# Kernel optimization log

Hardware: AMD Instinct MI355X
Metric: run time of the kernel (lower is better)

## Reference

```python
import jax, jax.numpy as jnp
import numpy as np

B, DIM, H, W = 8, 64, 64, 64
N_EMBED = 512
NNZ = 4          # num_nonzero OMP iterations
REG = 1e-7       # tiny Tikhonov term for the batched normal-equation solves


def batch_omp(X, D, S):
    """Batch OMP: for each signal pick S atoms greedily and solve LS on support.
    X: [N, d] signals, D: [d, K] dictionary with unit-norm atoms.
    Returns dense sparse code [N, K] with <= S nonzeros per row.
    Mathematically equivalent to the incremental-Cholesky Batch_OMP: at each
    step we solve G_II gamma = alpha0_I on the current support I.
    """
    N, K = X.shape[0], D.shape[1]
    G = D.T @ D                 # [K, K] Gram matrix (precomputed once)
    alpha0 = X @ D              # [N, K] initial correlations D^T x
    alpha = alpha0
    idx_cols = []
    gamma = None
    idx = None
    for k in range(S):          # static small loop over sparsity level
        j = jnp.argmax(jnp.abs(alpha), axis=1)                # [N] greedy atom
        idx_cols.append(j)
        idx = jnp.stack(idx_cols, axis=1)                     # [N, k+1]
        G_sub = G[idx[:, :, None], idx[:, None, :]]           # [N, k+1, k+1]
        rhs = jnp.take_along_axis(alpha0, idx, axis=1)        # [N, k+1]
        reg = REG * jnp.eye(k + 1, dtype=G.dtype)
        gamma = jnp.linalg.solve(G_sub + reg, rhs[..., None])[..., 0]  # [N, k+1]
        # residual correlations: alpha = alpha0 - G[:, I] gamma  (G symmetric)
        alpha = alpha0 - jnp.einsum('nak,na->nk', G[idx], gamma)
    code = jnp.zeros((N, K), X.dtype).at[jnp.arange(N)[:, None], idx].set(gamma)
    return code


def setup_inputs() -> dict:
    key = jax.random.key(0)
    kx, kd = jax.random.split(key)
    x = jax.random.normal(kx, (B, DIM, H, W), dtype=jnp.float32)
    dictionary = jax.random.normal(kd, (DIM, N_EMBED), dtype=jnp.float32)
    return {"x": x, "dictionary": dictionary}


def reference(x, dictionary):
    perm = jnp.transpose(x, (0, 2, 3, 1))            # [B, H, W, C]
    flat = perm.reshape(-1, DIM)                     # [N, C], N = B*H*W
    # normalize_dict=True: atoms normalized to unit L2 norm (in-place in torch)
    Dn = dictionary / jnp.linalg.norm(dictionary, axis=0, keepdims=True)
    code = batch_omp(flat, Dn, NNZ)                  # [N, K] (torch keeps [K, N])
    quant = (code @ Dn.T).reshape(perm.shape)        # reconstruction
    diff_enc = jnp.mean((quant - perm) ** 2)
    diff_dict = diff_enc                             # backward_dict=False branch
    # straight-through: perm + (quant - perm).detach() == quant in value
    out = jnp.transpose(quant, (0, 3, 1, 2))         # [B, C, H, W]
    ids = jnp.transpose(code.reshape(B, H, W, N_EMBED), (0, 3, 1, 2))  # [B, K, H, W]
    norm_0 = jnp.sum(code != 0, axis=1).astype(jnp.float32)  # L0 per signal, [N]
    num_steps = jnp.float32(NNZ)
    mean_D = jnp.mean(jnp.abs(Dn))
    mean_Z = jnp.mean(jnp.abs(code))
    norm_Z = jnp.mean(norm_0)
    topk_num = max(1, int(norm_0.shape[0] * 0.01))   # static: 327
    top_percentile = jnp.min(jax.lax.top_k(norm_0, topk_num)[0])
    num_zeros = jnp.sum(norm_0 == 0).astype(jnp.float32)
    return (out, diff_enc, diff_dict, ids, num_steps, mean_D, mean_Z,
            norm_Z, top_percentile, num_zeros)
```

## Files before the change

### kernel.cpp

```cpp
#include <hip/hip_runtime.h>
#include <cstdint>
#include <cstddef>

#define BQ 8
#define CDIM 64
#define HQ 64
#define WQ 64
#define KDIM 512
#define N_SIG 32768
#define S_NNZ 4

#define DIFF_ENC_OFF 2097152
#define DIFF_DICT_OFF 2097153
#define IDS_OFF 2097154
#define NUM_STEPS_OFF 18874370
#define MEAN_D_OFF 18874371
#define MEAN_Z_OFF 18874372
#define NORM_Z_OFF 18874373
#define TOP_PCT_OFF 18874374
#define NUM_ZEROS_OFF 18874375

#define WS_DN 16
#define WS_DNT 32784
#define WS_G 65552
#define WS_WG 327696
#define WS_WI 458768

__global__ __launch_bounds__(512) void k_dict(const float* __restrict__ D,
                                              float* __restrict__ Dn,
                                              float* __restrict__ DnT,
                                              float* __restrict__ W) {
  int tid = threadIdx.x;
  if (tid < 16) ((unsigned int*)W)[tid] = 0u;
  __syncthreads();
  double* accs = (double*)W;
  int k = tid;
  float ss = 0.f;
  for (int c = 0; c < CDIM; ++c) {
    float v = D[c * KDIM + k];
    ss = fmaf(v, v, ss);
  }
  float nrm = sqrtf(ss);
  float sabs = 0.f;
  for (int c = 0; c < CDIM; ++c) {
    float v = D[c * KDIM + k] / nrm;
    Dn[c * KDIM + k] = v;
    DnT[k * CDIM + c] = v;
    sabs += fabsf(v);
  }
#pragma unroll
  for (int off = 32; off >= 1; off >>= 1) sabs += __shfl_xor(sabs, off);
  if ((tid & 63) == 0) atomicAdd(&accs[0], (double)sabs);
}

__global__ __launch_bounds__(256) void k_gram(const float* __restrict__ Dn,
                                              float* __restrict__ G) {
  int g = blockIdx.x * 256 + threadIdx.x;
  int i = g >> 9, j = g & 511;
  float s = 0.f;
#pragma unroll 8
  for (int c = 0; c < CDIM; ++c) s = fmaf(Dn[c * KDIM + i], Dn[c * KDIM + j], s);
  G[(size_t)i * KDIM + j] = s;
}

__global__ __launch_bounds__(256) void k_alpha0(const float* __restrict__ X,
                                                const float* __restrict__ Dn,
                                                float* __restrict__ A0) {
  __shared__ float Xs[64 * 65];
  __shared__ float Dns[64 * 64];
  int tid = threadIdx.x;
  int mt = blockIdx.x >> 3, nt = blockIdx.x & 7;
  int b = mt >> 6, h = mt & 63;
  int w = tid & 63, cq = tid >> 6;
#pragma unroll
  for (int p = 0; p < 16; ++p) {
    int c = p * 4 + cq;
    Xs[w * 65 + c] = X[(((size_t)b * CDIM + c) * HQ + h) * WQ + w];
    Dns[c * 64 + w] = Dn[(size_t)c * KDIM + nt * 64 + w];
  }
  __syncthreads();
  int ty = tid >> 4, tx = tid & 15;
  float acc[4][4] = {};
  for (int c = 0; c < 64; ++c) {
    float av[4];
#pragma unroll
    for (int i = 0; i < 4; ++i) av[i] = Xs[(ty * 4 + i) * 65 + c];
    float4 bv = *(const float4*)&Dns[c * 64 + tx * 4];
#pragma unroll
    for (int i = 0; i < 4; ++i) {
      acc[i][0] = fmaf(av[i], bv.x, acc[i][0]);
      acc[i][1] = fmaf(av[i], bv.y, acc[i][1]);
      acc[i][2] = fmaf(av[i], bv.z, acc[i][2]);
      acc[i][3] = fmaf(av[i], bv.w, acc[i][3]);
    }
  }
  size_t n0 = (size_t)mt * 64;
#pragma unroll
  for (int i = 0; i < 4; ++i) {
    float4 st = make_float4(acc[i][0], acc[i][1], acc[i][2], acc[i][3]);
    *(float4*)&A0[(n0 + ty * 4 + i) * KDIM + nt * 64 + tx * 4] = st;
  }
}

template <int SZ>
__device__ __forceinline__ void solve_sz(const float (&gs)[4][4], const float (&rhs)[4],
                                         float (&gamma)[4]) {
  float M[SZ][SZ];
  float y[SZ];
  float idg[SZ];
#pragma unroll
  for (int a = 0; a < SZ; ++a) {
    y[a] = rhs[a];
#pragma unroll
    for (int b = 0; b < SZ; ++b) M[a][b] = gs[a][b] + (a == b ? 1e-7f : 0.0f);
  }
#pragma unroll
  for (int p = 0; p < SZ; ++p) {
    float ip = __builtin_amdgcn_rcpf(M[p][p]);
    idg[p] = ip;
#pragma unroll
    for (int r = p + 1; r < SZ; ++r) {
      float f = M[r][p] * ip;
#pragma unroll
      for (int c = p + 1; c < SZ; ++c) M[r][c] = fmaf(-f, M[p][c], M[r][c]);
      y[r] = fmaf(-f, y[p], y[r]);
    }
  }
#pragma unroll
  for (int r = SZ - 1; r >= 0; --r) {
    float t = y[r];
#pragma unroll
    for (int c = r + 1; c < SZ; ++c) t = fmaf(-M[r][c], gamma[c], t);
    gamma[r] = t * idg[r];
  }
}

template <int K>
__device__ __forceinline__ void omp_step(int lane, int n, const float* __restrict__ G,
                                         const float* __restrict__ A0,
                                         float (&a0)[8], float (&al)[8], float (&Grow)[4][8],
                                         float (&gs)[4][4], float (&rhs)[4], int (&idx)[4],
                                         float (&gamma)[4]) {
  float mx = fabsf(al[0]);
#pragma unroll
  for (int m = 1; m < 8; ++m) mx = fmaxf(mx, fabsf(al[m]));
#pragma unroll
  for (int off = 32; off >= 1; off >>= 1) mx = fmaxf(mx, __shfl_xor(mx, off));
  int mmask = 0;
#pragma unroll
  for (int m = 0; m < 8; ++m) mmask |= (fabsf(al[m]) == mx) ? (1 << m) : 0;
  unsigned long long ball = __ballot(mmask != 0);
  int srcl = (int)__builtin_ctzll(ball);
  int bm = __builtin_ctz((unsigned)__shfl(mmask, srcl) | 0x100u);
  int sk = __builtin_amdgcn_readfirstlane(srcl * 8 + bm);
  idx[K] = sk;

  const float4* gp = (const float4*)(G + (size_t)sk * KDIM + lane * 8);
  float4 r0 = gp[0], r1 = gp[1];
  Grow[K][0] = r0.x; Grow[K][1] = r0.y; Grow[K][2] = r0.z; Grow[K][3] = r0.w;
  Grow[K][4] = r1.x; Grow[K][5] = r1.y; Grow[K][6] = r1.z; Grow[K][7] = r1.w;

  const float* grow_base = G + (size_t)sk * KDIM;
#pragma unroll
  for (int b = 0; b < K; ++b) {
    float v = grow_base[idx[b]];
    gs[K][b] = v;
    gs[b][K] = v;
  }
  gs[K][K] = grow_base[sk];
  rhs[K] = A0[(size_t)n * KDIM + sk];

  solve_sz<K + 1>(gs, rhs, gamma);

  if (K < 3) {
#pragma unroll
    for (int m = 0; m < 8; ++m) {
      float acc = a0[m];
#pragma unroll
      for (int a = 0; a <= K; ++a) acc = fmaf(-gamma[a], Grow[a][m], acc);
      al[m] = acc;
    }
  }
}

__global__ __launch_bounds__(256) void k_omp(const float* __restrict__ A0,
                                             const float* __restrict__ G,
                                             float4* __restrict__ wg, int4* __restrict__ wi) {
  int tid = threadIdx.x;
  int lane = tid & 63;
  int wv = __builtin_amdgcn_readfirstlane(tid >> 6);
  int n = blockIdx.x * 4 + wv;
  const float4* ap = (const float4*)(A0 + (size_t)n * KDIM + lane * 8);
  float4 v0 = ap[0], v1 = ap[1];
  float a0[8] = {v0.x, v0.y, v0.z, v0.w, v1.x, v1.y, v1.z, v1.w};
  float al[8];
#pragma unroll
  for (int m = 0; m < 8; ++m) al[m] = a0[m];
  float Grow[4][8];
  float gs[4][4];
  float rhs[4];
  int idx[4];
  float gamma[4];
  omp_step<0>(lane, n, G, A0, a0, al, Grow, gs, rhs, idx, gamma);
  omp_step<1>(lane, n, G, A0, a0, al, Grow, gs, rhs, idx, gamma);
  omp_step<2>(lane, n, G, A0, a0, al, Grow, gs, rhs, idx, gamma);
  omp_step<3>(lane, n, G, A0, a0, al, Grow, gs, rhs, idx, gamma);
  bool k0 = (idx[0] != idx[1]) && (idx[0] != idx[2]) && (idx[0] != idx[3]);
  bool k1 = (idx[1] != idx[2]) && (idx[1] != idx[3]);
  bool k2 = (idx[2] != idx[3]);
  if (lane == 0) {
    wg[n] = make_float4(k0 ? gamma[0] : 0.f, k1 ? gamma[1] : 0.f,
                        k2 ? gamma[2] : 0.f, gamma[3]);
    wi[n] = make_int4(idx[0], idx[1], idx[2], idx[3]);
  }
}

__global__ __launch_bounds__(256) void k_epi(const float* __restrict__ X,
                                             const float* __restrict__ DnT,
                                             const float4* __restrict__ wg,
                                             const int4* __restrict__ wi,
                                             float* __restrict__ out, double* __restrict__ accs,
                                             int* __restrict__ hist) {
  __shared__ int sIdx[64][4];
  __shared__ float sKg[64][4];
  __shared__ float q[64 * 65];
  __shared__ float red[4];
  int tid = threadIdx.x;
  int bh = blockIdx.x;
  int b = bh >> 6, h = bh & 63;

  if (tid < 64) {
    int w = tid;
    int n = bh * 64 + w;
    int4 iv = wi[n];
    float4 gv = wg[n];
    sIdx[w][0] = iv.x; sIdx[w][1] = iv.y; sIdx[w][2] = iv.z; sIdx[w][3] = iv.w;
    sKg[w][0] = gv.x; sKg[w][1] = gv.y; sKg[w][2] = gv.z; sKg[w][3] = gv.w;
    int nz = (int)(gv.x != 0.f) + (int)(gv.y != 0.f) +
             (int)(gv.z != 0.f) + (int)(gv.w != 0.f);
    float s = fabsf(gv.x) + fabsf(gv.y) + fabsf(gv.z) + fabsf(gv.w);
#pragma unroll
    for (int off = 32; off >= 1; off >>= 1) s += __shfl_xor(s, off);
#pragma unroll
    for (int v = 0; v < 5; ++v) {
      unsigned long long m = __ballot(nz == v);
      if (tid == 0) {
        int c = (int)__popcll(m);
        if (c) atomicAdd(&hist[v], c);
      }
    }
    if (tid == 0) atomicAdd(&accs[1], (double)s);
  }
  __syncthreads();

  int w2 = tid & 63, p = tid >> 6, c0 = p * 16;
  float acc[16] = {};
#pragma unroll
  for (int s = 0; s < 4; ++s) {
    int ks = sIdx[w2][s];
    float g = sKg[w2][s];
    const float4* dp = (const float4*)(DnT + (size_t)ks * CDIM + c0);
#pragma unroll
    for (int i4 = 0; i4 < 4; ++i4) {
      float4 d = dp[i4];
      acc[i4 * 4 + 0] = fmaf(g, d.x, acc[i4 * 4 + 0]);
      acc[i4 * 4 + 1] = fmaf(g, d.y, acc[i4 * 4 + 1]);
      acc[i4 * 4 + 2] = fmaf(g, d.z, acc[i4 * 4 + 2]);
      acc[i4 * 4 + 3] = fmaf(g, d.w, acc[i4 * 4 + 3]);
    }
  }
#pragma unroll
  for (int i = 0; i < 16; ++i) q[(c0 + i) * 65 + w2] = acc[i];
  __syncthreads();

  float sumsq = 0.f;
#pragma unroll
  for (int pass = 0; pass < 16; ++pass) {
    int c = pass * 4 + p;
    float qv = q[c * 65 + w2];
    size_t off = (((size_t)b * CDIM + c) * HQ + h) * WQ + w2;
    float xv = X[off];
    float d = qv - xv;
    sumsq = fmaf(d, d, sumsq);
    out[off] = qv;
  }

#pragma unroll
  for (int off = 32; off >= 1; off >>= 1) sumsq += __shfl_xor(sumsq, off);
  if ((tid & 63) == 0) red[tid >> 6] = sumsq;
  __syncthreads();
  if (tid == 0) atomicAdd(&accs[2], (double)(red[0] + red[1] + red[2] + red[3]));
}

__global__ __launch_bounds__(256) void k_ids(const float4* __restrict__ wg,
                                             const int4* __restrict__ wi,
                                             float* __restrict__ out) {
  __shared__ int4 sIdx[64];
  __shared__ float4 sKg[64];
  int tid = threadIdx.x;
  int bh = blockIdx.x >> 2, kq = blockIdx.x & 3;
  int b = bh >> 6, h = bh & 63;
  if (tid < 64) {
    int n = bh * 64 + tid;
    sIdx[tid] = wi[n];
    sKg[tid] = wg[n];
  }
  __syncthreads();
  int w = tid & 63, kp = tid >> 6;
  int4 iv = sIdx[w];
  float4 gv = sKg[w];
  int k0 = kq * 128 + kp * 32;
  float* ids = out + IDS_OFF;
  size_t base = (((size_t)b * KDIM + k0) * HQ + h) * WQ + w;
#pragma unroll
  for (int kk = 0; kk < 32; ++kk) {
    int k = k0 + kk;
    float v = 0.f;
    v = (k == iv.x) ? gv.x : v;
    v = (k == iv.y) ? gv.y : v;
    v = (k == iv.z) ? gv.z : v;
    v = (k == iv.w) ? gv.w : v;
    ids[base + (size_t)kk * HQ * WQ] = v;
  }
}

__global__ __launch_bounds__(64) void k_final(const double* __restrict__ accs,
                                              const int* __restrict__ hist,
                                              float* __restrict__ out) {
  if (threadIdx.x == 0) {
    double sumAbsD = accs[0], sumAbsZ = accs[1], sumSq = accs[2];
    float diff = (float)(sumSq / 2097152.0);
    out[DIFF_ENC_OFF] = diff;
    out[DIFF_DICT_OFF] = diff;
    out[NUM_STEPS_OFF] = 4.0f;
    out[MEAN_D_OFF] = (float)(sumAbsD / 32768.0);
    out[MEAN_Z_OFF] = (float)(sumAbsZ / 16777216.0);
    int h0 = hist[0], h1 = hist[1], h2 = hist[2], h3 = hist[3], h4 = hist[4];
    out[NORM_Z_OFF] = (float)((double)(h1 + 2 * h2 + 3 * h3 + 4 * h4) / 32768.0);
    int cum = 0, res = 0;
    for (int v = 4; v >= 0; --v) {
      cum += hist[v];
      if (cum >= 327) { res = v; break; }
    }
    out[TOP_PCT_OFF] = (float)res;
    out[NUM_ZEROS_OFF] = (float)h0;
  }
}

extern "C" void kernel_launch(void* const* d_in, const int* in_sizes, int n_in,
                              void* d_out, int out_size, void* d_ws, size_t ws_size,
                              hipStream_t stream) {
  (void)in_sizes; (void)n_in; (void)out_size; (void)ws_size;
  const float* X = (const float*)d_in[0];
  const float* D = (const float*)d_in[1];
  float* out = (float*)d_out;
  float* W = (float*)d_ws;
  double* accs = (double*)d_ws;
  int* hist = (int*)W + 8;
  float* Dn = W + WS_DN;
  float* DnT = W + WS_DNT;
  float* G = W + WS_G;
  float4* wgam = (float4*)(W + WS_WG);
  int4* widx = (int4*)(W + WS_WI);
  float* A0 = out;

  hipLaunchKernelGGL(k_dict, dim3(1), dim3(512), 0, stream, D, Dn, DnT, W);
  hipLaunchKernelGGL(k_gram, dim3(1024), dim3(256), 0, stream, Dn, G);
  hipLaunchKernelGGL(k_alpha0, dim3(4096), dim3(256), 0, stream, X, Dn, A0);
  hipLaunchKernelGGL(k_omp, dim3(8192), dim3(256), 0, stream, A0, G, wgam, widx);
  hipLaunchKernelGGL(k_epi, dim3(512), dim3(256), 0, stream, X, DnT, wgam, widx, out, accs, hist);
  hipLaunchKernelGGL(k_ids, dim3(2048), dim3(256), 0, stream, wgam, widx, out);
  hipLaunchKernelGGL(k_final, dim3(1), dim3(64), 0, stream, accs, hist, out);
}
```

Before: 190.2 us.

## Merge gram/alpha0 and epilogue/ids kernels, parallelize dict norm, trim OMP work

Fuses the Gram-matrix computation into the alpha0 GEMM kernel as extra blocks and merges the epilogue and ids-scatter kernels into one launch. This cuts the launch count from seven to five. It also spreads dictionary normalization over 8 blocks, writing per-block partial sums instead of doing double atomics, and switches the tiled GEMMs to packed 2-wide FMA. In the OMP kernel it replaces the ballot/shuffle argmax with a per-element ballot loop and skips loading the G row on the last step. The fused kernels' branchy block split adds imbalance, and mean_D is now accumulated in float rather than double.

```diff
diff --git a/kernel.cpp b/kernel.cpp
--- a/kernel.cpp
+++ b/kernel.cpp
@@ -20,21 +20,21 @@
 #define TOP_PCT_OFF 18874374
 #define NUM_ZEROS_OFF 18874375
 
-#define WS_DN 16
-#define WS_DNT 32784
-#define WS_G 65552
-#define WS_WG 327696
-#define WS_WI 458768
-
-__global__ __launch_bounds__(512) void k_dict(const float* __restrict__ D,
-                                              float* __restrict__ Dn,
-                                              float* __restrict__ DnT,
-                                              float* __restrict__ W) {
+#define WS_PD 16
+#define WS_DN 32
+#define WS_DNT 32800
+#define WS_G 65568
+#define WS_WG 327712
+#define WS_WI 458784
+
+typedef float v2f __attribute__((ext_vector_type(2)));
+
+__global__ __launch_bounds__(64) void k_dict(const float* __restrict__ D,
+                                             float* __restrict__ Dn,
+                                             float* __restrict__ DnT,
+                                             float* __restrict__ pd) {
   int tid = threadIdx.x;
-  if (tid < 16) ((unsigned int*)W)[tid] = 0u;
-  __syncthreads();
-  double* accs = (double*)W;
-  int k = tid;
+  int k = blockIdx.x * 64 + tid;
   float ss = 0.f;
   for (int c = 0; c < CDIM; ++c) {
     float v = D[c * KDIM + k];
@@ -50,55 +50,80 @@
   }
 #pragma unroll
   for (int off = 32; off >= 1; off >>= 1) sabs += __shfl_xor(sabs, off);
-  if ((tid & 63) == 0) atomicAdd(&accs[0], (double)sabs);
-}
-
-__global__ __launch_bounds__(256) void k_gram(const float* __restrict__ Dn,
-                                              float* __restrict__ G) {
-  int g = blockIdx.x * 256 + threadIdx.x;
-  int i = g >> 9, j = g & 511;
-  float s = 0.f;
-#pragma unroll 8
-  for (int c = 0; c < CDIM; ++c) s = fmaf(Dn[c * KDIM + i], Dn[c * KDIM + j], s);
-  G[(size_t)i * KDIM + j] = s;
-}
-
-__global__ __launch_bounds__(256) void k_alpha0(const float* __restrict__ X,
-                                                const float* __restrict__ Dn,
-                                                float* __restrict__ A0) {
+  if (tid == 0) pd[blockIdx.x] = sabs;
+}
+
+__global__ __launch_bounds__(256) void k_ga(const float* __restrict__ X,
+                                            const float* __restrict__ Dn,
+                                            float* __restrict__ A0,
+                                            float* __restrict__ G,
+                                            float* __restrict__ W) {
   __shared__ float Xs[64 * 65];
   __shared__ float Dns[64 * 64];
   int tid = threadIdx.x;
-  int mt = blockIdx.x >> 3, nt = blockIdx.x & 7;
-  int b = mt >> 6, h = mt & 63;
   int w = tid & 63, cq = tid >> 6;
-#pragma unroll
-  for (int p = 0; p < 16; ++p) {
-    int c = p * 4 + cq;
-    Xs[w * 65 + c] = X[(((size_t)b * CDIM + c) * HQ + h) * WQ + w];
-    Dns[c * 64 + w] = Dn[(size_t)c * KDIM + nt * 64 + w];
-  }
-  __syncthreads();
   int ty = tid >> 4, tx = tid & 15;
-  float acc[4][4] = {};
-  for (int c = 0; c < 64; ++c) {
-    float av[4];
-#pragma unroll
-    for (int i = 0; i < 4; ++i) av[i] = Xs[(ty * 4 + i) * 65 + c];
-    float4 bv = *(const float4*)&Dns[c * 64 + tx * 4];
+
+  if (blockIdx.x < 64) {
+    if (blockIdx.x == 0 && tid < 16) ((unsigned int*)W)[tid] = 0u;
+    int ti = blockIdx.x >> 3, tj = blockIdx.x & 7;
+#pragma unroll
+    for (int p = 0; p < 16; ++p) {
+      int c = p * 4 + cq;
+      Xs[c * 64 + w] = Dn[(size_t)c * KDIM + ti * 64 + w];
+      Dns[c * 64 + w] = Dn[(size_t)c * KDIM + tj * 64 + w];
+    }
+    __syncthreads();
+    v2f acc[4][2] = {};
+    for (int c = 0; c < 64; ++c) {
+      float av[4];
+#pragma unroll
+      for (int i = 0; i < 4; ++i) av[i] = Xs[c * 64 + ty * 4 + i];
+      float4 bv = *(const float4*)&Dns[c * 64 + tx * 4];
+      v2f b0 = {bv.x, bv.y}, b1 = {bv.z, bv.w};
+#pragma unroll
+      for (int i = 0; i < 4; ++i) {
+        v2f a2 = {av[i], av[i]};
+        acc[i][0] = __builtin_elementwise_fma(a2, b0, acc[i][0]);
+        acc[i][1] = __builtin_elementwise_fma(a2, b1, acc[i][1]);
+      }
+    }
 #pragma unroll
     for (int i = 0; i < 4; ++i) {
-      acc[i][0] = fmaf(av[i], bv.x, acc[i][0]);
-      acc[i][1] = fmaf(av[i], bv.y, acc[i][1]);
-      acc[i][2] = fmaf(av[i], bv.z, acc[i][2]);
-      acc[i][3] = fmaf(av[i], bv.w, acc[i][3]);
-    }
-  }
-  size_t n0 = (size_t)mt * 64;
-#pragma unroll
-  for (int i = 0; i < 4; ++i) {
-    float4 st = make_float4(acc[i][0], acc[i][1], acc[i][2], acc[i][3]);
-    *(float4*)&A0[(n0 + ty * 4 + i) * KDIM + nt * 64 + tx * 4] = st;
+      float4 st = make_float4(acc[i][0].x, acc[i][0].y, acc[i][1].x, acc[i][1].y);
+      *(float4*)&G[(size_t)(ti * 64 + ty * 4 + i) * KDIM + tj * 64 + tx * 4] = st;
+    }
+  } else {
+    int bb = blockIdx.x - 64;
+    int mt = bb >> 3, nt = bb & 7;
+    int b = mt >> 6, h = mt & 63;
+#pragma unroll
+    for (int p = 0; p < 16; ++p) {
+      int c = p * 4 + cq;
+      Xs[w * 65 + c] = X[(((size_t)b * CDIM + c) * HQ + h) * WQ + w];
+      Dns[c * 64 + w] = Dn[(size_t)c * KDIM + nt * 64 + w];
+    }
+    __syncthreads();
+    v2f acc[4][2] = {};
+    for (int c = 0; c < 64; ++c) {
+      float av[4];
+#pragma unroll
+      for (int i = 0; i < 4; ++i) av[i] = Xs[(ty * 4 + i) * 65 + c];
+      float4 bv = *(const float4*)&Dns[c * 64 + tx * 4];
+      v2f b0 = {bv.x, bv.y}, b1 = {bv.z, bv.w};
+#pragma unroll
+      for (int i = 0; i < 4; ++i) {
+        v2f a2 = {av[i], av[i]};
+        acc[i][0] = __builtin_elementwise_fma(a2, b0, acc[i][0]);
+        acc[i][1] = __builtin_elementwise_fma(a2, b1, acc[i][1]);
+      }
+    }
+    size_t n0 = (size_t)mt * 64;
+#pragma unroll
+    for (int i = 0; i < 4; ++i) {
+      float4 st = make_float4(acc[i][0].x, acc[i][0].y, acc[i][1].x, acc[i][1].y);
+      *(float4*)&A0[(n0 + ty * 4 + i) * KDIM + nt * 64 + tx * 4] = st;
+    }
   }
 }
 
@@ -138,7 +163,7 @@
 template <int K>
 __device__ __forceinline__ void omp_step(int lane, int n, const float* __restrict__ G,
                                          const float* __restrict__ A0,
-                                         float (&a0)[8], float (&al)[8], float (&Grow)[4][8],
+                                         float (&a0)[8], float (&al)[8], float (&Grow)[3][8],
                                          float (&gs)[4][4], float (&rhs)[4], int (&idx)[4],
                                          float (&gamma)[4]) {
   float mx = fabsf(al[0]);
@@ -146,21 +171,25 @@
   for (int m = 1; m < 8; ++m) mx = fmaxf(mx, fabsf(al[m]));
 #pragma unroll
   for (int off = 32; off >= 1; off >>= 1) mx = fmaxf(mx, __shfl_xor(mx, off));
-  int mmask = 0;
-#pragma unroll
-  for (int m = 0; m < 8; ++m) mmask |= (fabsf(al[m]) == mx) ? (1 << m) : 0;
-  unsigned long long ball = __ballot(mmask != 0);
-  int srcl = (int)__builtin_ctzll(ball);
-  int bm = __builtin_ctz((unsigned)__shfl(mmask, srcl) | 0x100u);
-  int sk = __builtin_amdgcn_readfirstlane(srcl * 8 + bm);
+  int sk = 1 << 30;
+#pragma unroll
+  for (int m = 0; m < 8; ++m) {
+    unsigned long long bm = __ballot(fabsf(al[m]) == mx);
+    if (bm) {
+      int kk = (int)__builtin_ctzll(bm) * 8 + m;
+      sk = kk < sk ? kk : sk;
+    }
+  }
   idx[K] = sk;
 
-  const float4* gp = (const float4*)(G + (size_t)sk * KDIM + lane * 8);
-  float4 r0 = gp[0], r1 = gp[1];
-  Grow[K][0] = r0.x; Grow[K][1] = r0.y; Grow[K][2] = r0.z; Grow[K][3] = r0.w;
-  Grow[K][4] = r1.x; Grow[K][5] = r1.y; Grow[K][6] = r1.z; Grow[K][7] = r1.w;
-
   const float* grow_base = G + (size_t)sk * KDIM;
+  if constexpr (K < 3) {
+    const float4* gp = (const float4*)(grow_base + lane * 8);
+    float4 r0 = gp[0], r1 = gp[1];
+    Grow[K][0] = r0.x; Grow[K][1] = r0.y; Grow[K][2] = r0.z; Grow[K][3] = r0.w;
+    Grow[K][4] = r1.x; Grow[K][5] = r1.y; Grow[K][6] = r1.z; Grow[K][7] = r1.w;
+  }
+
 #pragma unroll
   for (int b = 0; b < K; ++b) {
     float v = grow_base[idx[b]];
@@ -172,7 +201,7 @@
 
   solve_sz<K + 1>(gs, rhs, gamma);
 
-  if (K < 3) {
+  if constexpr (K < 3) {
 #pragma unroll
     for (int m = 0; m < 8; ++m) {
       float acc = a0[m];
@@ -196,7 +225,7 @@
   float al[8];
 #pragma unroll
   for (int m = 0; m < 8; ++m) al[m] = a0[m];
-  float Grow[4][8];
+  float Grow[3][8];
   float gs[4][4];
   float rhs[4];
   int idx[4];
@@ -215,125 +244,125 @@
   }
 }
 
-__global__ __launch_bounds__(256) void k_epi(const float* __restrict__ X,
-                                             const float* __restrict__ DnT,
-                                             const float4* __restrict__ wg,
-                                             const int4* __restrict__ wi,
-                                             float* __restrict__ out, double* __restrict__ accs,
-                                             int* __restrict__ hist) {
-  __shared__ int sIdx[64][4];
-  __shared__ float sKg[64][4];
+__global__ __launch_bounds__(256) void k_ei(const float* __restrict__ X,
+                                            const float* __restrict__ DnT,
+                                            const float4* __restrict__ wg,
+                                            const int4* __restrict__ wi,
+                                            float* __restrict__ out, double* __restrict__ accs,
+                                            int* __restrict__ hist) {
+  __shared__ __align__(16) int sIdx[64][4];
+  __shared__ __align__(16) float sKg[64][4];
   __shared__ float q[64 * 65];
   __shared__ float red[4];
   int tid = threadIdx.x;
-  int bh = blockIdx.x;
-  int b = bh >> 6, h = bh & 63;
-
-  if (tid < 64) {
-    int w = tid;
-    int n = bh * 64 + w;
-    int4 iv = wi[n];
-    float4 gv = wg[n];
-    sIdx[w][0] = iv.x; sIdx[w][1] = iv.y; sIdx[w][2] = iv.z; sIdx[w][3] = iv.w;
-    sKg[w][0] = gv.x; sKg[w][1] = gv.y; sKg[w][2] = gv.z; sKg[w][3] = gv.w;
-    int nz = (int)(gv.x != 0.f) + (int)(gv.y != 0.f) +
-             (int)(gv.z != 0.f) + (int)(gv.w != 0.f);
-    float s = fabsf(gv.x) + fabsf(gv.y) + fabsf(gv.z) + fabsf(gv.w);
-#pragma unroll
-    for (int off = 32; off >= 1; off >>= 1) s += __shfl_xor(s, off);
-#pragma unroll
-    for (int v = 0; v < 5; ++v) {
-      unsigned long long m = __ballot(nz == v);
-      if (tid == 0) {
-        int c = (int)__popcll(m);
-        if (c) atomicAdd(&hist[v], c);
+
+  if (blockIdx.x < 512) {
+    int bh = blockIdx.x;
+    int b = bh >> 6, h = bh & 63;
+    if (tid < 64) {
+      int w = tid;
+      int n = bh * 64 + w;
+      int4 iv = wi[n];
+      float4 gv = wg[n];
+      sIdx[w][0] = iv.x; sIdx[w][1] = iv.y; sIdx[w][2] = iv.z; sIdx[w][3] = iv.w;
+      sKg[w][0] = gv.x; sKg[w][1] = gv.y; sKg[w][2] = gv.z; sKg[w][3] = gv.w;
+      int nz = (int)(gv.x != 0.f) + (int)(gv.y != 0.f) +
+               (int)(gv.z != 0.f) + (int)(gv.w != 0.f);
+      float s = fabsf(gv.x) + fabsf(gv.y) + fabsf(gv.z) + fabsf(gv.w);
+#pragma unroll
+      for (int off = 32; off >= 1; off >>= 1) s += __shfl_xor(s, off);
+#pragma unroll
+      for (int v = 0; v < 5; ++v) {
+        unsigned long long m = __ballot(nz == v);
+        if (tid == 0) {
+          int c = (int)__popcll(m);
+          if (c) atomicAdd(&hist[v], c);
+        }
       }
-    }
-    if (tid == 0) atomicAdd(&accs[1], (double)s);
-  }
-  __syncthreads();
-
-  int w2 = tid & 63, p = tid >> 6, c0 = p * 16;
-  float acc[16] = {};
-#pragma unroll
-  for (int s = 0; s < 4; ++s) {
-    int ks = sIdx[w2][s];
-    float g = sKg[w2][s];
-    const float4* dp = (const float4*)(DnT + (size_t)ks * CDIM + c0);
-#pragma unroll
-    for (int i4 = 0; i4 < 4; ++i4) {
-      float4 d = dp[i4];
-      acc[i4 * 4 + 0] = fmaf(g, d.x, acc[i4 * 4 + 0]);
-      acc[i4 * 4 + 1] = fmaf(g, d.y, acc[i4 * 4 + 1]);
-      acc[i4 * 4 + 2] = fmaf(g, d.z, acc[i4 * 4 + 2]);
-      acc[i4 * 4 + 3] = fmaf(g, d.w, acc[i4 * 4 + 3]);
-    }
-  }
-#pragma unroll
-  for (int i = 0; i < 16; ++i) q[(c0 + i) * 65 + w2] = acc[i];
-  __syncthreads();
-
-  float sumsq = 0.f;
-#pragma unroll
-  for (int pass = 0; pass < 16; ++pass) {
-    int c = pass * 4 + p;
-    float qv = q[c * 65 + w2];
-    size_t off = (((size_t)b * CDIM + c) * HQ + h) * WQ + w2;
-    float xv = X[off];
-    float d = qv - xv;
-    sumsq = fmaf(d, d, sumsq);
-    out[off] = qv;
-  }
-
-#pragma unroll
-  for (int off = 32; off >= 1; off >>= 1) sumsq += __shfl_xor(sumsq, off);
-  if ((tid & 63) == 0) red[tid >> 6] = sumsq;
-  __syncthreads();
-  if (tid == 0) atomicAdd(&accs[2], (double)(red[0] + red[1] + red[2] + red[3]));
-}
-
-__global__ __launch_bounds__(256) void k_ids(const float4* __restrict__ wg,
-                                             const int4* __restrict__ wi,
-                                             float* __restrict__ out) {
-  __shared__ int4 sIdx[64];
-  __shared__ float4 sKg[64];
-  int tid = threadIdx.x;
-  int bh = blockIdx.x >> 2, kq = blockIdx.x & 3;
-  int b = bh >> 6, h = bh & 63;
-  if (tid < 64) {
-    int n = bh * 64 + tid;
-    sIdx[tid] = wi[n];
-    sKg[tid] = wg[n];
-  }
-  __syncthreads();
-  int w = tid & 63, kp = tid >> 6;
-  int4 iv = sIdx[w];
-  float4 gv = sKg[w];
-  int k0 = kq * 128 + kp * 32;
-  float* ids = out + IDS_OFF;
-  size_t base = (((size_t)b * KDIM + k0) * HQ + h) * WQ + w;
-#pragma unroll
-  for (int kk = 0; kk < 32; ++kk) {
-    int k = k0 + kk;
-    float v = 0.f;
-    v = (k == iv.x) ? gv.x : v;
-    v = (k == iv.y) ? gv.y : v;
-    v = (k == iv.z) ? gv.z : v;
-    v = (k == iv.w) ? gv.w : v;
-    ids[base + (size_t)kk * HQ * WQ] = v;
+      if (tid == 0) atomicAdd(&accs[0], (double)s);
+    }
+    __syncthreads();
+
+    int w2 = tid & 63, p = tid >> 6, c0 = p * 16;
+    float acc[16] = {};
+#pragma unroll
+    for (int s = 0; s < 4; ++s) {
+      int ks = sIdx[w2][s];
+      float g = sKg[w2][s];
+      const float4* dp = (const float4*)(DnT + (size_t)ks * CDIM + c0);
+#pragma unroll
+      for (int i4 = 0; i4 < 4; ++i4) {
+        float4 d = dp[i4];
+        acc[i4 * 4 + 0] = fmaf(g, d.x, acc[i4 * 4 + 0]);
+        acc[i4 * 4 + 1] = fmaf(g, d.y, acc[i4 * 4 + 1]);
+        acc[i4 * 4 + 2] = fmaf(g, d.z, acc[i4 * 4 + 2]);
+        acc[i4 * 4 + 3] = fmaf(g, d.w, acc[i4 * 4 + 3]);
+      }
+    }
+#pragma unroll
+    for (int i = 0; i < 16; ++i) q[(c0 + i) * 65 + w2] = acc[i];
+    __syncthreads();
+
+    float sumsq = 0.f;
+#pragma unroll
+    for (int pass = 0; pass < 16; ++pass) {
+      int c = pass * 4 + p;
+      float qv = q[c * 65 + w2];
+      size_t off = (((size_t)b * CDIM + c) * HQ + h) * WQ + w2;
+      float xv = X[off];
+      float d = qv - xv;
+      sumsq = fmaf(d, d, sumsq);
+      out[off] = qv;
+    }
+
+#pragma unroll
+    for (int off = 32; off >= 1; off >>= 1) sumsq += __shfl_xor(sumsq, off);
+    if ((tid & 63) == 0) red[tid >> 6] = sumsq;
+    __syncthreads();
+    if (tid == 0) atomicAdd(&accs[1], (double)(red[0] + red[1] + red[2] + red[3]));
+  } else {
+    int bid = blockIdx.x - 512;
+    int bh = bid >> 2, kq = bid & 3;
+    int b = bh >> 6, h = bh & 63;
+    if (tid < 64) {
+      int n = bh * 64 + tid;
+      *(int4*)&sIdx[tid][0] = wi[n];
+      *(float4*)&sKg[tid][0] = wg[n];
+    }
+    __syncthreads();
+    int w = tid & 63, kp = tid >> 6;
+    int4 iv = *(int4*)&sIdx[w][0];
+    float4 gv = *(float4*)&sKg[w][0];
+    int k0 = kq * 128 + kp * 32;
+    float* ids = out + IDS_OFF;
+    size_t base = (((size_t)b * KDIM + k0) * HQ + h) * WQ + w;
+#pragma unroll
+    for (int kk = 0; kk < 32; ++kk) {
+      int k = k0 + kk;
+      float v = 0.f;
+      v = (k == iv.x) ? gv.x : v;
+      v = (k == iv.y) ? gv.y : v;
+      v = (k == iv.z) ? gv.z : v;
+      v = (k == iv.w) ? gv.w : v;
+      ids[base + (size_t)kk * HQ * WQ] = v;
+    }
   }
 }
 
 __global__ __launch_bounds__(64) void k_final(const double* __restrict__ accs,
                                               const int* __restrict__ hist,
+                                              const float* __restrict__ pd,
                                               float* __restrict__ out) {
   if (threadIdx.x == 0) {
-    double sumAbsD = accs[0], sumAbsZ = accs[1], sumSq = accs[2];
+    float sumAbsD = 0.f;
+#pragma unroll
+    for (int i = 0; i < 8; ++i) sumAbsD += pd[i];
+    double sumAbsZ = accs[0], sumSq = accs[1];
     float diff = (float)(sumSq / 2097152.0);
     out[DIFF_ENC_OFF] = diff;
     out[DIFF_DICT_OFF] = diff;
     out[NUM_STEPS_OFF] = 4.0f;
-    out[MEAN_D_OFF] = (float)(sumAbsD / 32768.0);
+    out[MEAN_D_OFF] = sumAbsD / 32768.0f;
     out[MEAN_Z_OFF] = (float)(sumAbsZ / 16777216.0);
     int h0 = hist[0], h1 = hist[1], h2 = hist[2], h3 = hist[3], h4 = hist[4];
     out[NORM_Z_OFF] = (float)((double)(h1 + 2 * h2 + 3 * h3 + 4 * h4) / 32768.0);
@@ -356,7 +385,8 @@
   float* out = (float*)d_out;
   float* W = (float*)d_ws;
   double* accs = (double*)d_ws;
-  int* hist = (int*)W + 8;
+  int* hist = (int*)W + 4;
+  float* pd = W + WS_PD;
   float* Dn = W + WS_DN;
   float* DnT = W + WS_DNT;
   float* G = W + WS_G;
@@ -364,11 +394,9 @@
   int4* widx = (int4*)(W + WS_WI);
   float* A0 = out;
 
-  hipLaunchKernelGGL(k_dict, dim3(1), dim3(512), 0, stream, D, Dn, DnT, W);
-  hipLaunchKernelGGL(k_gram, dim3(1024), dim3(256), 0, stream, Dn, G);
-  hipLaunchKernelGGL(k_alpha0, dim3(4096), dim3(256), 0, stream, X, Dn, A0);
+  hipLaunchKernelGGL(k_dict, dim3(8), dim3(64), 0, stream, D, Dn, DnT, pd);
+  hipLaunchKernelGGL(k_ga, dim3(4160), dim3(256), 0, stream, X, Dn, A0, G, W);
   hipLaunchKernelGGL(k_omp, dim3(8192), dim3(256), 0, stream, A0, G, wgam, widx);
-  hipLaunchKernelGGL(k_epi, dim3(512), dim3(256), 0, stream, X, DnT, wgam, widx, out, accs, hist);
-  hipLaunchKernelGGL(k_ids, dim3(2048), dim3(256), 0, stream, wgam, widx, out);
-  hipLaunchKernelGGL(k_final, dim3(1), dim3(64), 0, stream, accs, hist, out);
-}
+  hipLaunchKernelGGL(k_ei, dim3(2560), dim3(256), 0, stream, X, DnT, wgam, widx, out, accs, hist);
+  hipLaunchKernelGGL(k_final, dim3(1), dim3(64), 0, stream, accs, hist, pd, out);
+}
```

Result: faster. 171.7 us (-9.7%).
